# Kernel tuning notes

Hardware: AMD Instinct MI355X
Metric: run time of the kernel (lower is better)

Reference implementation:

```python
import jax, jax.numpy as jnp
import numpy as np

B, J, K, M, D = 64, 8, 64, 32, 256
TEMP = 0.1
EPS = 1e-8  # torch CosineSimilarity eps
NUM_LABELS = 16


def setup_inputs() -> dict:
    key = jax.random.key(0)
    k1, k2, k3, k4, k5 = jax.random.split(key, 5)
    return {
        "childrens": jax.random.normal(k1, (B, J, D), jnp.float32),
        "childrens_pos": jax.random.normal(k2, (B, J, D), jnp.float32),
        "childrens_negs": jax.random.normal(k3, (B, K, M, D), jnp.float32),
        "childrens_gt_labels": jax.random.randint(k4, (B, J), 0, NUM_LABELS),
        "childrens_gt_label_negs": jax.random.randint(k5, (B, K, M), 0, NUM_LABELS),
    }


def _cos(a, b):
    # cosine similarity over last axis with torch-style eps clamping
    na = jnp.maximum(jnp.linalg.norm(a, axis=-1), EPS)
    nb = jnp.maximum(jnp.linalg.norm(b, axis=-1), EPS)
    return jnp.sum(a * b, axis=-1) / (na * nb)


def reference(childrens, childrens_pos, childrens_negs, childrens_gt_labels, childrens_gt_label_negs):
    # Faithful to the original indentation bug: only the LAST child (j = J-1)
    # of each group i contributes to the loss.
    Bn = childrens.shape[0]
    child = childrens[:, -1]                    # [B, D]
    pos = childrens_pos[:, -1]                  # [B, D]
    label = childrens_gt_labels[:, -1]          # [B]

    negs = childrens_negs.reshape(Bn, -1, childrens_negs.shape[-1])   # [B, K*M, D]
    neg_labels = childrens_gt_label_negs.reshape(Bn, -1)              # [B, K*M]

    pos_sim = _cos(child, pos) / TEMP                                 # [B]
    neg_sim = _cos(child[:, None, :], negs) / TEMP                    # [B, K*M]

    # Only negatives whose gt label equals the child's label are included;
    # excluded ones get -inf so they vanish from the CE partition function.
    mask = neg_labels == label[:, None]
    neg_sim = jnp.where(mask, neg_sim, -jnp.inf)

    logits = jnp.concatenate([pos_sim[:, None], neg_sim], axis=1)     # [B, 1+K*M]
    # CrossEntropyLoss(reduction='sum') with target class 0
    loss = jax.nn.logsumexp(logits, axis=1) - pos_sim                 # [B]
    return jnp.sum(loss) / (2 * Bn)
```

## Files before the change

### kernel.cpp

```cpp
#include <hip/hip_runtime.h>
#include <math.h>

constexpr int B = 64, J = 8, K = 64, M = 32, D = 256;
constexpr int NNEG = K * M;
constexpr float TEMP = 0.1f;
constexpr float EPS = 1e-8f;
constexpr float SHIFT = 10.0f;

constexpr int SLICES = 8;
constexpr int NEG_PER_BLOCK = NNEG / SLICES;
constexpr int NBLK = B * SLICES;

__global__ __launch_bounds__(256) void neg_partial_kernel(
    const float* __restrict__ childrens,
    const float* __restrict__ childrens_pos,
    const int*   __restrict__ gt_labels,
    const float* __restrict__ negs,
    const int*   __restrict__ neg_labels,
    float*       __restrict__ partials,
    float*       __restrict__ pos_sims) {
  const int blk  = blockIdx.x;
  const int b    = blk / SLICES;
  const int s    = blk % SLICES;
  const int tid  = threadIdx.x;
  const int lane = tid & 63;
  const int wave = tid >> 6;

  __shared__ float child_hat[D];
  __shared__ float red[4];
  __shared__ float redpp[4];
  __shared__ float redcp[4];

  const float* child = childrens + ((size_t)b * J + (J - 1)) * D;
  float cv = child[tid];
  float ss = cv * cv;
  #pragma unroll
  for (int off = 32; off > 0; off >>= 1) ss += __shfl_down(ss, off, 64);
  if (lane == 0) red[wave] = ss;
  __syncthreads();
  const float norm2 = red[0] + red[1] + red[2] + red[3];
  const float inv_n = 1.0f / fmaxf(sqrtf(norm2), EPS);
  child_hat[tid] = cv * inv_n;
  __syncthreads();

  const int label = gt_labels[b * J + (J - 1)];

  const int neg_base = s * NEG_PER_BLOCK + wave * 64;
  const int*   nl      = neg_labels + (size_t)b * NNEG;
  const float* nv_base = negs + (size_t)b * NNEG * D;

  const float4 ch = ((const float4*)child_hat)[lane];

  const int nlab = nl[neg_base + lane];
  unsigned long long mask = __ballot(nlab == label);

  float acc = 0.0f;
  while (mask) {
    int idx[4];
    int cnt = 0;
    idx[0] = __ffsll((long long)mask) - 1;
    mask &= mask - 1;
    cnt = 1;
    #pragma unroll
    for (int t = 1; t < 4; ++t) {
      if (mask) {
        idx[t] = __ffsll((long long)mask) - 1;
        mask &= mask - 1;
        ++cnt;
      } else {
        idx[t] = idx[0];
      }
    }

    float dot[4], nn[4];
    #pragma unroll
    for (int t = 0; t < 4; ++t) {
      const float4* nv =
          (const float4*)(nv_base + (size_t)(neg_base + idx[t]) * D);
      const float4 x = nv[lane];
      dot[t] = ch.x * x.x + ch.y * x.y + ch.z * x.z + ch.w * x.w;
      nn[t]  = x.x * x.x + x.y * x.y + x.z * x.z + x.w * x.w;
    }
    #pragma unroll
    for (int off = 32; off > 0; off >>= 1) {
      #pragma unroll
      for (int t = 0; t < 4; ++t) {
        dot[t] += __shfl_down(dot[t], off, 64);
        nn[t]  += __shfl_down(nn[t],  off, 64);
      }
    }
    if (lane == 0) {
      #pragma unroll
      for (int t = 0; t < 4; ++t) {
        if (t < cnt) {
          const float sim = dot[t] / (fmaxf(sqrtf(nn[t]), EPS) * TEMP);
          acc += expf(sim - SHIFT);
        }
      }
    }
  }

  if (s == 0) {
    const float* pos = childrens_pos + ((size_t)b * J + (J - 1)) * D;
    const float pv = pos[tid];
    float pp = pv * pv;
    float cp = child_hat[tid] * pv;
    #pragma unroll
    for (int off = 32; off > 0; off >>= 1) {
      pp += __shfl_down(pp, off, 64);
      cp += __shfl_down(cp, off, 64);
    }
    if (lane == 0) { redpp[wave] = pp; redcp[wave] = cp; }
  }

  if (lane == 0) red[wave] = acc;
  __syncthreads();
  if (tid == 0) {
    float total = red[0] + red[1] + red[2] + red[3];
    if (s == 0) {
      const float ppt = redpp[0] + redpp[1] + redpp[2] + redpp[3];
      const float cpt = redcp[0] + redcp[1] + redcp[2] + redcp[3];
      const float pos_sim = cpt / (fmaxf(sqrtf(ppt), EPS) * TEMP);
      pos_sims[b] = pos_sim;
      total += expf(pos_sim - SHIFT);
    }
    partials[blk] = total;
  }
}

__global__ __launch_bounds__(64) void finalize_kernel(
    const float* __restrict__ partials,
    const float* __restrict__ pos_sims,
    float*       __restrict__ out) {
  const int lane = threadIdx.x;
  float sum = 0.0f;
  #pragma unroll
  for (int t = 0; t < SLICES; ++t) sum += partials[lane * SLICES + t];
  const float ps = pos_sims[lane];
  float loss = logf(sum) + SHIFT - ps;
  #pragma unroll
  for (int off = 32; off > 0; off >>= 1) loss += __shfl_down(loss, off, 64);
  if (lane == 0) out[0] = loss / (2.0f * B);
}

extern "C" void kernel_launch(void* const* d_in, const int* in_sizes, int n_in,
                              void* d_out, int out_size, void* d_ws, size_t ws_size,
                              hipStream_t stream) {
  const float* childrens      = (const float*)d_in[0];
  const float* childrens_pos  = (const float*)d_in[1];
  const float* childrens_negs = (const float*)d_in[2];
  const int*   gt_labels      = (const int*)d_in[3];
  const int*   gt_label_negs  = (const int*)d_in[4];
  float* out = (float*)d_out;

  float* partials = (float*)d_ws;
  float* pos_sims = partials + NBLK;

  neg_partial_kernel<<<NBLK, 256, 0, stream>>>(
      childrens, childrens_pos, gt_labels, childrens_negs, gt_label_negs,
      partials, pos_sims);
  finalize_kernel<<<1, 64, 0, stream>>>(partials, pos_sims, out);
}
```

Measured before the change: 178.0 us.

## Fuse finalize into main kernel via atomics and last-wave reduction, drop block syncs

Folds the finalize kernel into the main kernel. Each wave atomically adds its partial sum into a per-batch accumulator, and the last wave to arrive, detected with a global atomic counter, computes the final loss. The shared-memory child normalization and both __syncthreads are removed: each wave keeps the raw child vector in registers and applies the inverse norm as a scalar, and the positive similarity is computed by a single wave. A memset of the accumulators is added before launch. The cost is atomic contention and ordering that depends on fences.

```diff
diff --git a/kernel.cpp b/kernel.cpp
--- a/kernel.cpp
+++ b/kernel.cpp
@@ -10,57 +10,52 @@
 constexpr int SLICES = 8;
 constexpr int NEG_PER_BLOCK = NNEG / SLICES;
 constexpr int NBLK = B * SLICES;
+constexpr int TOTAL_WAVES = NBLK * 4;
 
-__global__ __launch_bounds__(256) void neg_partial_kernel(
+__global__ __launch_bounds__(256) void ntxent_fused_kernel(
     const float* __restrict__ childrens,
     const float* __restrict__ childrens_pos,
     const int*   __restrict__ gt_labels,
     const float* __restrict__ negs,
     const int*   __restrict__ neg_labels,
-    float*       __restrict__ partials,
-    float*       __restrict__ pos_sims) {
+    float*       __restrict__ ws,
+    float*       __restrict__ out) {
   const int blk  = blockIdx.x;
-  const int b    = blk / SLICES;
-  const int s    = blk % SLICES;
+  const int b    = blk >> 3;
+  const int s    = blk & 7;
   const int tid  = threadIdx.x;
   const int lane = tid & 63;
   const int wave = tid >> 6;
 
-  __shared__ float child_hat[D];
-  __shared__ float red[4];
-  __shared__ float redpp[4];
-  __shared__ float redcp[4];
+  float* acc_buf  = ws;
+  float* possum_p = ws + B;
+  unsigned int* counter_p = (unsigned int*)(ws + B + 1);
 
   const float* child = childrens + ((size_t)b * J + (J - 1)) * D;
-  float cv = child[tid];
-  float ss = cv * cv;
+  const float4 cv = ((const float4*)child)[lane];
+  const int label = gt_labels[b * J + (J - 1)];
+  const int neg_base = s * NEG_PER_BLOCK + wave * 64;
+  const int nlab = neg_labels[(size_t)b * NNEG + neg_base + lane];
+
+  float4 pv = make_float4(0.f, 0.f, 0.f, 0.f);
+  const bool do_pos = (s == 0) && (wave == 0);
+  if (do_pos)
+    pv = ((const float4*)(childrens_pos + ((size_t)b * J + (J - 1)) * D))[lane];
+
+  float ss = cv.x * cv.x + cv.y * cv.y + cv.z * cv.z + cv.w * cv.w;
   #pragma unroll
   for (int off = 32; off > 0; off >>= 1) ss += __shfl_down(ss, off, 64);
-  if (lane == 0) red[wave] = ss;
-  __syncthreads();
-  const float norm2 = red[0] + red[1] + red[2] + red[3];
-  const float inv_n = 1.0f / fmaxf(sqrtf(norm2), EPS);
-  child_hat[tid] = cv * inv_n;
-  __syncthreads();
 
-  const int label = gt_labels[b * J + (J - 1)];
-
-  const int neg_base = s * NEG_PER_BLOCK + wave * 64;
-  const int*   nl      = neg_labels + (size_t)b * NNEG;
   const float* nv_base = negs + (size_t)b * NNEG * D;
-
-  const float4 ch = ((const float4*)child_hat)[lane];
-
-  const int nlab = nl[neg_base + lane];
   unsigned long long mask = __ballot(nlab == label);
 
   float acc = 0.0f;
+  const float cn_inv_t = 1.0f / (fmaxf(sqrtf(ss), EPS) * TEMP);
   while (mask) {
     int idx[4];
-    int cnt = 0;
+    int cnt = 1;
     idx[0] = __ffsll((long long)mask) - 1;
     mask &= mask - 1;
-    cnt = 1;
     #pragma unroll
     for (int t = 1; t < 4; ++t) {
       if (mask) {
@@ -75,10 +70,9 @@
     float dot[4], nn[4];
     #pragma unroll
     for (int t = 0; t < 4; ++t) {
-      const float4* nv =
-          (const float4*)(nv_base + (size_t)(neg_base + idx[t]) * D);
-      const float4 x = nv[lane];
-      dot[t] = ch.x * x.x + ch.y * x.y + ch.z * x.z + ch.w * x.w;
+      const float4 x =
+          ((const float4*)(nv_base + (size_t)(neg_base + idx[t]) * D))[lane];
+      dot[t] = cv.x * x.x + cv.y * x.y + cv.z * x.z + cv.w * x.w;
       nn[t]  = x.x * x.x + x.y * x.y + x.z * x.z + x.w * x.w;
     }
     #pragma unroll
@@ -93,54 +87,47 @@
       #pragma unroll
       for (int t = 0; t < 4; ++t) {
         if (t < cnt) {
-          const float sim = dot[t] / (fmaxf(sqrtf(nn[t]), EPS) * TEMP);
+          const float sim = dot[t] * cn_inv_t / fmaxf(sqrtf(nn[t]), EPS);
           acc += expf(sim - SHIFT);
         }
       }
     }
   }
 
-  if (s == 0) {
-    const float* pos = childrens_pos + ((size_t)b * J + (J - 1)) * D;
-    const float pv = pos[tid];
-    float pp = pv * pv;
-    float cp = child_hat[tid] * pv;
+  if (do_pos) {
+    float pp = pv.x * pv.x + pv.y * pv.y + pv.z * pv.z + pv.w * pv.w;
+    float cp = cv.x * pv.x + cv.y * pv.y + cv.z * pv.z + cv.w * pv.w;
     #pragma unroll
     for (int off = 32; off > 0; off >>= 1) {
       pp += __shfl_down(pp, off, 64);
       cp += __shfl_down(cp, off, 64);
     }
-    if (lane == 0) { redpp[wave] = pp; redcp[wave] = cp; }
+    if (lane == 0) {
+      const float pos_sim = cp * cn_inv_t / fmaxf(sqrtf(pp), EPS);
+      acc += expf(pos_sim - SHIFT);
+      atomicAdd(possum_p, pos_sim);
+    }
   }
 
-  if (lane == 0) red[wave] = acc;
-  __syncthreads();
-  if (tid == 0) {
-    float total = red[0] + red[1] + red[2] + red[3];
-    if (s == 0) {
-      const float ppt = redpp[0] + redpp[1] + redpp[2] + redpp[3];
-      const float cpt = redcp[0] + redcp[1] + redcp[2] + redcp[3];
-      const float pos_sim = cpt / (fmaxf(sqrtf(ppt), EPS) * TEMP);
-      pos_sims[b] = pos_sim;
-      total += expf(pos_sim - SHIFT);
+  unsigned int old = 0;
+  if (lane == 0) {
+    if (acc != 0.0f) atomicAdd(acc_buf + b, acc);
+    __threadfence();
+    old = atomicAdd(counter_p, 1u);
+  }
+  old = (unsigned int)__shfl((int)old, 0, 64);
+
+  if (old == TOTAL_WAVES - 1) {
+    __threadfence();
+    const float a = atomicAdd(acc_buf + lane, 0.0f);
+    float l = logf(a);
+    #pragma unroll
+    for (int off = 32; off > 0; off >>= 1) l += __shfl_down(l, off, 64);
+    if (lane == 0) {
+      const float psum = atomicAdd(possum_p, 0.0f);
+      out[0] = (l + (float)B * SHIFT - psum) / (2.0f * B);
     }
-    partials[blk] = total;
   }
-}
-
-__global__ __launch_bounds__(64) void finalize_kernel(
-    const float* __restrict__ partials,
-    const float* __restrict__ pos_sims,
-    float*       __restrict__ out) {
-  const int lane = threadIdx.x;
-  float sum = 0.0f;
-  #pragma unroll
-  for (int t = 0; t < SLICES; ++t) sum += partials[lane * SLICES + t];
-  const float ps = pos_sims[lane];
-  float loss = logf(sum) + SHIFT - ps;
-  #pragma unroll
-  for (int off = 32; off > 0; off >>= 1) loss += __shfl_down(loss, off, 64);
-  if (lane == 0) out[0] = loss / (2.0f * B);
 }
 
 extern "C" void kernel_launch(void* const* d_in, const int* in_sizes, int n_in,
@@ -152,12 +139,11 @@
   const int*   gt_labels      = (const int*)d_in[3];
   const int*   gt_label_negs  = (const int*)d_in[4];
   float* out = (float*)d_out;
+  float* ws  = (float*)d_ws;
 
-  float* partials = (float*)d_ws;
-  float* pos_sims = partials + NBLK;
+  hipMemsetAsync(d_ws, 0, (B + 2) * sizeof(float), stream);
 
-  neg_partial_kernel<<<NBLK, 256, 0, stream>>>(
+  ntxent_fused_kernel<<<NBLK, 256, 0, stream>>>(
       childrens, childrens_pos, gt_labels, childrens_negs, gt_label_negs,
-      partials, pos_sims);
-  finalize_kernel<<<1, 64, 0, stream>>>(partials, pos_sims, out);
+      ws, out);
 }
```

Result: slower. 224.5 us (+26.1%).
